# Kernel tuning notes

Measured on AMD Instinct MI355X. Metric: run time of the kernel, lower is better.

The kernel has to match this reference:

```python
import jax, jax.numpy as jnp
import numpy as np

MAX_POS = 1024  # max_position_embeddings


def setup_inputs() -> dict:
    key = jax.random.key(0)
    k1, k2, k3 = jax.random.split(key, 3)
    B, H, S, D = 2, 16, 1024, 64
    E = H * D  # embed_size = 1024
    query = jax.random.normal(k1, (B, H, S, D), dtype=jnp.float32)
    position_embeddings = jax.random.normal(k2, (2 * MAX_POS - 1, E), dtype=jnp.float32)
    dense_kernel = jax.random.normal(k3, (E, E), dtype=jnp.float32) * 0.02
    return {"query": query, "position_embeddings": position_embeddings, "dense_kernel": dense_kernel}


def _gather_pos_embedding(position_embeddings, seq_length):
    # indices max_pos - S .. max_pos + S - 2, clamped to [0, 2*max_pos - 2]
    idx = jnp.arange(MAX_POS - seq_length, MAX_POS + seq_length - 1)
    max_id = 2 * MAX_POS - 2
    idx = jnp.clip(idx, 0, max_id)  # same effect as the sign-mask clamping in the TF code
    return position_embeddings[idx]  # [2S-1, E]


def reference(query, position_embeddings, dense_kernel):
    B, H, S, D = query.shape
    emb = _gather_pos_embedding(position_embeddings, S)          # [2S-1, E]
    emb = emb @ dense_kernel                                      # Dense, no bias: [2S-1, E]
    emb = emb.reshape(-1, H, D).transpose(1, 0, 2)                # [H, 2S-1, D]
    q = query.reshape(H, -1, D)                                   # faithful raw reshape: [H, B*S, D]
    score = jnp.einsum('hnd,hmd->hnm', q, emb)                    # [H, B*S, 2S-1]
    # Transformer-XL style relative shift via computed flat indices
    rel = jnp.arange(S - 1, 2 * S - 1)[None, :] - jnp.arange(S)[:, None]
    rel = rel + jnp.arange(S)[:, None] * (2 * S - 1)              # [S, S] flat indices into S*(2S-1)
    rel = rel.reshape(-1)
    score = score.reshape(H, B, -1)                               # [H, B, S*(2S-1)]
    score = jnp.take(score, rel, axis=2)                          # [H, B, S*S]
    return score.reshape(B, H, S, S)                              # faithful raw reshape
```

## Files before the change

kernel.cpp:

```cpp
#include <hip/hip_runtime.h>

typedef __bf16 bf16;
typedef __bf16 bf16x4 __attribute__((ext_vector_type(4)));
typedef __bf16 bf16x8 __attribute__((ext_vector_type(8)));
typedef float f32x4 __attribute__((ext_vector_type(4)));

#define SEQ 1024
#define EMB 1024
#define NH 16
#define HD 64
#define M2 2047

__global__ __launch_bounds__(256) void gemm1_kernel(const float* __restrict__ posEmb,
                                                    const float* __restrict__ W,
                                                    bf16* __restrict__ P) {
  __shared__ bf16 As[64][72];
  __shared__ bf16 Bs[64][72];
  const int tid  = threadIdx.x;
  const int lane = tid & 63;
  const int wave = tid >> 6;
  const int wr = wave >> 1, wc = wave & 1;
  const int m0 = blockIdx.y * 64;
  const int n0 = blockIdx.x * 64;

  f32x4 acc[2][2] = {};

  for (int k0 = 0; k0 < EMB; k0 += 64) {
    {
      const int row = tid >> 2;
      const int c0  = (tid & 3) * 16;
      int g = m0 + row;
      if (g > M2 - 1) g = M2 - 1;
      const float4* src = reinterpret_cast<const float4*>(posEmb + (size_t)g * EMB + k0 + c0);
      #pragma unroll
      for (int i = 0; i < 4; ++i) {
        float4 v = src[i];
        bf16x4 bb = { (bf16)v.x, (bf16)v.y, (bf16)v.z, (bf16)v.w };
        *reinterpret_cast<bf16x4*>(&As[row][c0 + 4 * i]) = bb;
      }
    }
    {
      const int n  = tid & 63;
      const int kg = tid >> 6;
      #pragma unroll
      for (int u = 0; u < 4; ++u) {
        bf16x4 bb;
        #pragma unroll
        for (int e = 0; e < 4; ++e) {
          int k = kg * 16 + u * 4 + e;
          bb[e] = (bf16)W[(size_t)(k0 + k) * EMB + n0 + n];
        }
        *reinterpret_cast<bf16x4*>(&Bs[n][kg * 16 + u * 4]) = bb;
      }
    }
    __syncthreads();
    #pragma unroll
    for (int ks = 0; ks < 2; ++ks) {
      bf16x8 a[2], b[2];
      #pragma unroll
      for (int x = 0; x < 2; ++x) {
        a[x] = *reinterpret_cast<const bf16x8*>(&As[wr * 32 + x * 16 + (lane & 15)][ks * 32 + 8 * (lane >> 4)]);
        b[x] = *reinterpret_cast<const bf16x8*>(&Bs[wc * 32 + x * 16 + (lane & 15)][ks * 32 + 8 * (lane >> 4)]);
      }
      #pragma unroll
      for (int x = 0; x < 2; ++x)
        #pragma unroll
        for (int y = 0; y < 2; ++y)
          acc[x][y] = __builtin_amdgcn_mfma_f32_16x16x32_bf16(a[x], b[y], acc[x][y], 0, 0, 0);
    }
    __syncthreads();
  }

  #pragma unroll
  for (int x = 0; x < 2; ++x)
    #pragma unroll
    for (int y = 0; y < 2; ++y)
      #pragma unroll
      for (int r = 0; r < 4; ++r) {
        int row = m0 + wr * 32 + x * 16 + (lane >> 4) * 4 + r;
        int col = n0 + wc * 32 + y * 16 + (lane & 15);
        P[(size_t)row * EMB + col] = (bf16)acc[x][y][r];
      }
}

__global__ __launch_bounds__(256) void band2_kernel(const float* __restrict__ q,
                                                    const bf16* __restrict__ P,
                                                    float* __restrict__ out) {
  __shared__ bf16 Pbuf[2][64 * 64];
  const int tid  = threadIdx.x;
  const int lane = tid & 63;
  const int wave = tid >> 6;
  const int wr = wave >> 1, wc = wave & 1;

  const int i0 = blockIdx.x * 64;
  const int hb = blockIdx.y;
  const int h  = hb >> 1;
  const int b  = hb & 1;

  bf16x8 a[2][2];
  {
    const float* qbase = q + ((size_t)(h * (2 * SEQ) + b * SEQ)) * HD;
    const int row = i0 + wr * 32 + (lane & 15);
    const int kof = 8 * (lane >> 4);
    #pragma unroll
    for (int x = 0; x < 2; ++x)
      #pragma unroll
      for (int ks = 0; ks < 2; ++ks) {
        const float* src = qbase + (size_t)(row + x * 16) * HD + ks * 32 + kof;
        float4 v0 = *reinterpret_cast<const float4*>(src);
        float4 v1 = *reinterpret_cast<const float4*>(src + 4);
        bf16x8 f = { (bf16)v0.x, (bf16)v0.y, (bf16)v0.z, (bf16)v0.w,
                     (bf16)v1.x, (bf16)v1.y, (bf16)v1.z, (bf16)v1.w };
        a[x][ks] = f;
      }
  }

  const int m_base = (SEQ - 1) - (i0 + 63);
  const int tb = blockIdx.z * 9;
  const int te = (blockIdx.z == 0) ? 9 : 17;

  auto STAGE = [&](int bi, int t) {
    const int m0 = m_base + t * 64;
    const char* Pb = reinterpret_cast<const char*>(P);
    #pragma unroll
    for (int i = 0; i < 2; ++i) {
      int s   = wave * 128 + i * 64 + lane;
      int row = s >> 3;
      int cs  = s & 7;
      int cd  = cs ^ (row & 7);
      const void* g = Pb + ((size_t)(m0 + row) * EMB + h * HD) * 2 + cd * 16;
      char* l = reinterpret_cast<char*>(&Pbuf[bi][0]) + (wave * 128 + i * 64) * 16;
      __builtin_amdgcn_global_load_lds(
          (const __attribute__((address_space(1))) void*)g,
          (__attribute__((address_space(3))) void*)l, 16, 0, 0);
    }
  };

  const size_t outbase = (size_t)hb << 20;

  STAGE(0, tb);
  __syncthreads();

  int cur = 0;
  for (int t = tb; t < te; ++t) {
    if (t + 1 < te) STAGE(cur ^ 1, t + 1);

    const char* buf = reinterpret_cast<const char*>(&Pbuf[cur][0]);
    f32x4 acc[2][2] = {};
    #pragma unroll
    for (int ks = 0; ks < 2; ++ks) {
      bf16x8 bb[2];
      #pragma unroll
      for (int y = 0; y < 2; ++y) {
        int mrow  = wc * 32 + y * 16 + (lane & 15);
        int chunk = ks * 4 + (lane >> 4);
        int sw    = chunk ^ (mrow & 7);
        bb[y] = *reinterpret_cast<const bf16x8*>(buf + mrow * 128 + sw * 16);
      }
      #pragma unroll
      for (int x = 0; x < 2; ++x)
        #pragma unroll
        for (int y = 0; y < 2; ++y)
          acc[x][y] = __builtin_amdgcn_mfma_f32_16x16x32_bf16(a[x][ks], bb[y], acc[x][y], 0, 0, 0);
    }

    const int m0 = m_base + t * 64;
    #pragma unroll
    for (int x = 0; x < 2; ++x)
      #pragma unroll
      for (int y = 0; y < 2; ++y)
        #pragma unroll
        for (int r = 0; r < 4; ++r) {
          int i = i0 + wr * 32 + x * 16 + (lane >> 4) * 4 + r;
          int m = m0 + wc * 32 + y * 16 + (lane & 15);
          int j = m - (SEQ - 1) + i;
          if ((unsigned)j < SEQ)
            out[outbase + (size_t)i * SEQ + j] = acc[x][y][r];
        }

    __syncthreads();
    cur ^= 1;
  }
}

extern "C" void kernel_launch(void* const* d_in, const int* in_sizes, int n_in,
                              void* d_out, int out_size, void* d_ws, size_t ws_size,
                              hipStream_t stream) {
  const float* query  = (const float*)d_in[0];
  const float* posEmb = (const float*)d_in[1];
  const float* W      = (const float*)d_in[2];
  float* out = (float*)d_out;
  bf16* P = (bf16*)d_ws;

  gemm1_kernel<<<dim3(16, 32), 256, 0, stream>>>(posEmb, W, P);
  band2_kernel<<<dim3(16, 32, 2), 256, 0, stream>>>(query, P, out);
}
```

Measured before the change: 61.26 us.

## Pre-convert GEMM inputs to bf16 and pipeline GEMM with async LDS loads

Adds a prep kernel that converts the position embeddings to bf16 and writes a transposed bf16 copy of the dense weight into workspace. The GEMM then streams both operands with direct global-to-LDS loads into a double-buffered, XOR-swizzled shared-memory layout, replacing the per-iteration fp32 loads, conversions and strided column reads of W. The aim is to remove the uncoalesced weight access and overlap loads with MFMA work. The cost is an extra kernel launch and an extra round trip of the converted data through global memory.

```diff
diff --git a/kernel.cpp b/kernel.cpp
--- a/kernel.cpp
+++ b/kernel.cpp
@@ -11,11 +11,50 @@
 #define HD 64
 #define M2 2047
 
-__global__ __launch_bounds__(256) void gemm1_kernel(const float* __restrict__ posEmb,
-                                                    const float* __restrict__ W,
-                                                    bf16* __restrict__ P) {
-  __shared__ bf16 As[64][72];
-  __shared__ bf16 Bs[64][72];
+__global__ __launch_bounds__(256) void prep_kernel(const float* __restrict__ posEmb,
+                                                   const float* __restrict__ W,
+                                                   bf16* __restrict__ Ab,
+                                                   bf16* __restrict__ Wt) {
+  const int tid = threadIdx.x;
+  const int bx  = blockIdx.x;
+  if (bx < 256) {
+    __shared__ bf16 Tt[64][66];
+    const int k0 = (bx >> 4) * 64, n0 = (bx & 15) * 64;
+    const int r = tid >> 2, cb = (tid & 3) * 16;
+    const float4* src = reinterpret_cast<const float4*>(W + (size_t)(k0 + r) * EMB + n0 + cb);
+    #pragma unroll
+    for (int v = 0; v < 4; ++v) {
+      float4 f = src[v];
+      Tt[cb + v * 4 + 0][r] = (bf16)f.x;
+      Tt[cb + v * 4 + 1][r] = (bf16)f.y;
+      Tt[cb + v * 4 + 2][r] = (bf16)f.z;
+      Tt[cb + v * 4 + 3][r] = (bf16)f.w;
+    }
+    __syncthreads();
+    bf16* dst = Wt + (size_t)(n0 + r) * EMB + k0 + cb;
+    bf16x8 o0, o1;
+    #pragma unroll
+    for (int i = 0; i < 8; ++i) { o0[i] = Tt[r][cb + i]; o1[i] = Tt[r][cb + 8 + i]; }
+    *reinterpret_cast<bf16x8*>(dst)     = o0;
+    *reinterpret_cast<bf16x8*>(dst + 8) = o1;
+  } else {
+    const int idx = (bx - 256) * 256 + tid;
+    const int m = idx >> 7;
+    const int c = (idx & 127) * 8;
+    const int g = m > M2 - 1 ? M2 - 1 : m;
+    const float4* s = reinterpret_cast<const float4*>(posEmb + (size_t)g * EMB + c);
+    float4 v0 = s[0], v1 = s[1];
+    bf16x8 o = { (bf16)v0.x, (bf16)v0.y, (bf16)v0.z, (bf16)v0.w,
+                 (bf16)v1.x, (bf16)v1.y, (bf16)v1.z, (bf16)v1.w };
+    *reinterpret_cast<bf16x8*>(Ab + (size_t)m * EMB + c) = o;
+  }
+}
+
+__global__ __launch_bounds__(256) void gemm1b_kernel(const bf16* __restrict__ Ab,
+                                                     const bf16* __restrict__ Wt,
+                                                     bf16* __restrict__ P) {
+  __shared__ bf16 As[2][64 * 64];
+  __shared__ bf16 Bs[2][64 * 64];
   const int tid  = threadIdx.x;
   const int lane = tid & 63;
   const int wave = tid >> 6;
@@ -23,44 +62,50 @@
   const int m0 = blockIdx.y * 64;
   const int n0 = blockIdx.x * 64;
 
+  const char* AbB = reinterpret_cast<const char*>(Ab);
+  const char* WtB = reinterpret_cast<const char*>(Wt);
+
+  auto STAGE = [&](int bi, int k0) {
+    #pragma unroll
+    for (int i = 0; i < 2; ++i) {
+      int s   = wave * 128 + i * 64 + lane;
+      int row = s >> 3;
+      int cs  = s & 7;
+      int cd  = cs ^ (row & 7);
+      const void* ga = AbB + ((size_t)(m0 + row) * EMB + k0) * 2 + cd * 16;
+      const void* gb = WtB + ((size_t)(n0 + row) * EMB + k0) * 2 + cd * 16;
+      char* la = reinterpret_cast<char*>(&As[bi][0]) + s * 16;
+      char* lb = reinterpret_cast<char*>(&Bs[bi][0]) + s * 16;
+      __builtin_amdgcn_global_load_lds(
+          (const __attribute__((address_space(1))) void*)ga,
+          (__attribute__((address_space(3))) void*)la, 16, 0, 0);
+      __builtin_amdgcn_global_load_lds(
+          (const __attribute__((address_space(1))) void*)gb,
+          (__attribute__((address_space(3))) void*)lb, 16, 0, 0);
+    }
+  };
+
   f32x4 acc[2][2] = {};
 
-  for (int k0 = 0; k0 < EMB; k0 += 64) {
-    {
-      const int row = tid >> 2;
-      const int c0  = (tid & 3) * 16;
-      int g = m0 + row;
-      if (g > M2 - 1) g = M2 - 1;
-      const float4* src = reinterpret_cast<const float4*>(posEmb + (size_t)g * EMB + k0 + c0);
-      #pragma unroll
-      for (int i = 0; i < 4; ++i) {
-        float4 v = src[i];
-        bf16x4 bb = { (bf16)v.x, (bf16)v.y, (bf16)v.z, (bf16)v.w };
-        *reinterpret_cast<bf16x4*>(&As[row][c0 + 4 * i]) = bb;
-      }
-    }
-    {
-      const int n  = tid & 63;
-      const int kg = tid >> 6;
-      #pragma unroll
-      for (int u = 0; u < 4; ++u) {
-        bf16x4 bb;
-        #pragma unroll
-        for (int e = 0; e < 4; ++e) {
-          int k = kg * 16 + u * 4 + e;
-          bb[e] = (bf16)W[(size_t)(k0 + k) * EMB + n0 + n];
-        }
-        *reinterpret_cast<bf16x4*>(&Bs[n][kg * 16 + u * 4]) = bb;
-      }
-    }
-    __syncthreads();
+  STAGE(0, 0);
+  __syncthreads();
+
+  int cur = 0;
+  for (int t = 0; t < 16; ++t) {
+    if (t < 15) STAGE(cur ^ 1, (t + 1) * 64);
+
+    const char* bufA = reinterpret_cast<const char*>(&As[cur][0]);
+    const char* bufB = reinterpret_cast<const char*>(&Bs[cur][0]);
     #pragma unroll
     for (int ks = 0; ks < 2; ++ks) {
       bf16x8 a[2], b[2];
       #pragma unroll
       for (int x = 0; x < 2; ++x) {
-        a[x] = *reinterpret_cast<const bf16x8*>(&As[wr * 32 + x * 16 + (lane & 15)][ks * 32 + 8 * (lane >> 4)]);
-        b[x] = *reinterpret_cast<const bf16x8*>(&Bs[wc * 32 + x * 16 + (lane & 15)][ks * 32 + 8 * (lane >> 4)]);
+        int ra = wr * 32 + x * 16 + (lane & 15);
+        int rb = wc * 32 + x * 16 + (lane & 15);
+        int ch = ks * 4 + (lane >> 4);
+        a[x] = *reinterpret_cast<const bf16x8*>(bufA + ra * 128 + (ch ^ (ra & 7)) * 16);
+        b[x] = *reinterpret_cast<const bf16x8*>(bufB + rb * 128 + (ch ^ (rb & 7)) * 16);
       }
       #pragma unroll
       for (int x = 0; x < 2; ++x)
@@ -69,6 +114,7 @@
           acc[x][y] = __builtin_amdgcn_mfma_f32_16x16x32_bf16(a[x], b[y], acc[x][y], 0, 0, 0);
     }
     __syncthreads();
+    cur ^= 1;
   }
 
   #pragma unroll
@@ -190,8 +236,13 @@
   const float* posEmb = (const float*)d_in[1];
   const float* W      = (const float*)d_in[2];
   float* out = (float*)d_out;
-  bf16* P = (bf16*)d_ws;
-
-  gemm1_kernel<<<dim3(16, 32), 256, 0, stream>>>(posEmb, W, P);
+
+  char* ws = (char*)d_ws;
+  bf16* P  = (bf16*)(ws);
+  bf16* Ab = (bf16*)(ws + (4u << 20));
+  bf16* Wt = (bf16*)(ws + (8u << 20));
+
+  prep_kernel<<<1280, 256, 0, stream>>>(posEmb, W, Ab, Wt);
+  gemm1b_kernel<<<dim3(16, 32), 256, 0, stream>>>(Ab, Wt, P);
   band2_kernel<<<dim3(16, 32, 2), 256, 0, stream>>>(query, P, out);
 }
```

New measurement: 63.83 us. +4.2%, slower.

## Stage 16-row output slab in LDS and store coalesced float4 rows

Applied to the files above, without the earlier changes.

Restructures the banded score kernel so each block handles 16 query rows instead of 64, sweeping all 17 position tiles. Results go into a 64KB LDS slab, which is then written to global memory as contiguous float4 stores instead of scattered masked scalar stores. The aim is to cut uncoalesced write traffic on the large output. The cost is more position-tile loads per output row (about 2x redundant MFMA work over the band), a large LDS footprint that limits occupancy, and a tile-index clamp at the top row.

```diff
diff --git a/kernel.cpp b/kernel.cpp
--- a/kernel.cpp
+++ b/kernel.cpp
@@ -83,44 +83,37 @@
       }
 }
 
-__global__ __launch_bounds__(256) void band2_kernel(const float* __restrict__ q,
+__global__ __launch_bounds__(256) void band3_kernel(const float* __restrict__ q,
                                                     const bf16* __restrict__ P,
                                                     float* __restrict__ out) {
-  __shared__ bf16 Pbuf[2][64 * 64];
+  __shared__ float slab[16 * 1024];
+  __shared__ bf16  Pbuf[2][64 * 64];
   const int tid  = threadIdx.x;
   const int lane = tid & 63;
   const int wave = tid >> 6;
-  const int wr = wave >> 1, wc = wave & 1;
 
-  const int i0 = blockIdx.x * 64;
+  const int i0 = blockIdx.x * 16;
   const int hb = blockIdx.y;
   const int h  = hb >> 1;
   const int b  = hb & 1;
 
-  bf16x8 a[2][2];
+  bf16x8 a[2];
   {
-    const float* qbase = q + ((size_t)(h * (2 * SEQ) + b * SEQ)) * HD;
-    const int row = i0 + wr * 32 + (lane & 15);
-    const int kof = 8 * (lane >> 4);
+    const float* src0 = q + ((size_t)(h * (2 * SEQ) + b * SEQ + i0 + (lane & 15))) * HD;
     #pragma unroll
-    for (int x = 0; x < 2; ++x)
-      #pragma unroll
-      for (int ks = 0; ks < 2; ++ks) {
-        const float* src = qbase + (size_t)(row + x * 16) * HD + ks * 32 + kof;
-        float4 v0 = *reinterpret_cast<const float4*>(src);
-        float4 v1 = *reinterpret_cast<const float4*>(src + 4);
-        bf16x8 f = { (bf16)v0.x, (bf16)v0.y, (bf16)v0.z, (bf16)v0.w,
-                     (bf16)v1.x, (bf16)v1.y, (bf16)v1.z, (bf16)v1.w };
-        a[x][ks] = f;
-      }
+    for (int ks = 0; ks < 2; ++ks) {
+      const float* s = src0 + ks * 32 + 8 * (lane >> 4);
+      float4 v0 = *reinterpret_cast<const float4*>(s);
+      float4 v1 = *reinterpret_cast<const float4*>(s + 4);
+      bf16x8 f = { (bf16)v0.x, (bf16)v0.y, (bf16)v0.z, (bf16)v0.w,
+                   (bf16)v1.x, (bf16)v1.y, (bf16)v1.z, (bf16)v1.w };
+      a[ks] = f;
+    }
   }
 
-  const int m_base = (SEQ - 1) - (i0 + 63);
-  const int tb = blockIdx.z * 9;
-  const int te = (blockIdx.z == 0) ? 9 : 17;
+  const int m_base = (SEQ - 1) - (i0 + 15);
 
   auto STAGE = [&](int bi, int t) {
-    const int m0 = m_base + t * 64;
     const char* Pb = reinterpret_cast<const char*>(P);
     #pragma unroll
     for (int i = 0; i < 2; ++i) {
@@ -128,58 +121,53 @@
       int row = s >> 3;
       int cs  = s & 7;
       int cd  = cs ^ (row & 7);
-      const void* g = Pb + ((size_t)(m0 + row) * EMB + h * HD) * 2 + cd * 16;
-      char* l = reinterpret_cast<char*>(&Pbuf[bi][0]) + (wave * 128 + i * 64) * 16;
+      int gm  = m_base + t * 64 + row;
+      if (gm > M2) gm = M2;
+      const void* g = Pb + ((size_t)gm * EMB + h * HD) * 2 + cd * 16;
+      char* l = reinterpret_cast<char*>(&Pbuf[bi][0]) + s * 16;
       __builtin_amdgcn_global_load_lds(
           (const __attribute__((address_space(1))) void*)g,
           (__attribute__((address_space(3))) void*)l, 16, 0, 0);
     }
   };
 
-  const size_t outbase = (size_t)hb << 20;
-
-  STAGE(0, tb);
+  STAGE(0, 0);
   __syncthreads();
 
   int cur = 0;
-  for (int t = tb; t < te; ++t) {
-    if (t + 1 < te) STAGE(cur ^ 1, t + 1);
+  for (int t = 0; t < 17; ++t) {
+    if (t < 16) STAGE(cur ^ 1, t + 1);
 
     const char* buf = reinterpret_cast<const char*>(&Pbuf[cur][0]);
-    f32x4 acc[2][2] = {};
+    f32x4 acc = {};
     #pragma unroll
     for (int ks = 0; ks < 2; ++ks) {
-      bf16x8 bb[2];
-      #pragma unroll
-      for (int y = 0; y < 2; ++y) {
-        int mrow  = wc * 32 + y * 16 + (lane & 15);
-        int chunk = ks * 4 + (lane >> 4);
-        int sw    = chunk ^ (mrow & 7);
-        bb[y] = *reinterpret_cast<const bf16x8*>(buf + mrow * 128 + sw * 16);
-      }
-      #pragma unroll
-      for (int x = 0; x < 2; ++x)
-        #pragma unroll
-        for (int y = 0; y < 2; ++y)
-          acc[x][y] = __builtin_amdgcn_mfma_f32_16x16x32_bf16(a[x][ks], bb[y], acc[x][y], 0, 0, 0);
+      int mrow  = wave * 16 + (lane & 15);
+      int chunk = ks * 4 + (lane >> 4);
+      int sw    = chunk ^ (mrow & 7);
+      bf16x8 pb = *reinterpret_cast<const bf16x8*>(buf + mrow * 128 + sw * 16);
+      acc = __builtin_amdgcn_mfma_f32_16x16x32_bf16(a[ks], pb, acc, 0, 0, 0);
     }
 
     const int m0 = m_base + t * 64;
+    const int mloc = m0 + wave * 16 + (lane & 15);
     #pragma unroll
-    for (int x = 0; x < 2; ++x)
-      #pragma unroll
-      for (int y = 0; y < 2; ++y)
-        #pragma unroll
-        for (int r = 0; r < 4; ++r) {
-          int i = i0 + wr * 32 + x * 16 + (lane >> 4) * 4 + r;
-          int m = m0 + wc * 32 + y * 16 + (lane & 15);
-          int j = m - (SEQ - 1) + i;
-          if ((unsigned)j < SEQ)
-            out[outbase + (size_t)i * SEQ + j] = acc[x][y][r];
-        }
+    for (int r = 0; r < 4; ++r) {
+      int il = (lane >> 4) * 4 + r;
+      int j  = mloc - (SEQ - 1) + i0 + il;
+      if ((unsigned)j < SEQ) slab[il * SEQ + j] = acc[r];
+    }
 
     __syncthreads();
     cur ^= 1;
+  }
+
+  const size_t outb = ((size_t)hb << 20) + (size_t)i0 * SEQ;
+  #pragma unroll
+  for (int c = 0; c < 16; ++c) {
+    int flat = c * 1024 + tid * 4;
+    float4 v = *reinterpret_cast<const float4*>(&slab[flat]);
+    *reinterpret_cast<float4*>(&out[outb + flat]) = v;
   }
 }
 
@@ -193,5 +181,5 @@
   bf16* P = (bf16*)d_ws;
 
   gemm1_kernel<<<dim3(16, 32), 256, 0, stream>>>(posEmb, W, P);
-  band2_kernel<<<dim3(16, 32, 2), 256, 0, stream>>>(query, P, out);
+  band3_kernel<<<dim3(64, 32), 256, 0, stream>>>(query, P, out);
 }
```

Result: slower. 70.49 us (+15.1%).
